# Kernel optimization log

Hardware: AMD Instinct MI355X
Metric: run time of the kernel (lower is better)

The kernel has to match this reference:

```python
import jax, jax.numpy as jnp
import numpy as np

EPS = 1e-5


def conv2d(x, w, stride=1, pad=1, b=None):
    out = jax.lax.conv_general_dilated(
        x, w, (stride, stride), [(pad, pad), (pad, pad)],
        dimension_numbers=('NCHW', 'OIHW', 'NCHW'))
    if b is not None:
        out = out + b[None, :, None, None]
    return out


def batchnorm(x, g, b):
    # training-mode BN (torch default): batch statistics over (N, H, W)
    m = x.mean((0, 2, 3), keepdims=True)
    v = x.var((0, 2, 3), keepdims=True)
    return (x - m) * jax.lax.rsqrt(v + EPS) * g[None, :, None, None] + b[None, :, None, None]


def deform(x, w_off):
    # ConvOffset2D: learn (B, 2C, H, W) offsets, bilinearly resample x per channel.
    B, C, H, W = x.shape
    off = conv2d(x, w_off, 1, 1)                 # (B, 2C, H, W)
    off = off.reshape(B * C, H * W, 2)           # matches torch row-major view to (B*C, H, W, 2)
    ii, jj = jnp.meshgrid(jnp.arange(H), jnp.arange(W), indexing='ij')
    grid = jnp.stack([ii, jj], -1).reshape(H * W, 2).astype(x.dtype)
    coords = off + grid[None]                    # absolute sample coords
    ci = jnp.clip(coords[..., 0], 0.0, H - 1)
    cj = jnp.clip(coords[..., 1], 0.0, W - 1)
    i0 = jnp.floor(ci)
    i1 = jnp.ceil(ci)
    j0 = jnp.floor(cj)
    j1 = jnp.ceil(cj)
    xf = x.reshape(B * C, H * W)

    def gather(iy, jx):
        idx = (iy * W + jx).astype(jnp.int32)
        return jnp.take_along_axis(xf, idx, axis=1)

    v00 = gather(i0, j0)
    v10 = gather(i1, j0)
    v01 = gather(i0, j1)
    v11 = gather(i1, j1)
    di = ci - i0
    dj = cj - j0
    top = v00 + di * (v10 - v00)   # interpolate along rows
    bot = v01 + di * (v11 - v01)
    out = top + dj * (bot - top)   # then along cols
    return out.reshape(B, C, H, W)


def setup_inputs() -> dict:
    key = jax.random.key(0)
    ks = jax.random.split(key, 24)
    f32 = jnp.float32
    d = {
        'x': jax.random.normal(ks[0], (64, 1, 112, 112), dtype=f32),
        'w11': jax.random.normal(ks[1], (32, 1, 3, 3), dtype=f32) * 0.1,
        'b11': jnp.zeros((32,), f32),
        'g11': jnp.ones((32,), f32),
        'be11': jnp.zeros((32,), f32),
        'woff12': jax.random.normal(ks[2], (64, 32, 3, 3), dtype=f32) * 0.01,
        'w12': jax.random.normal(ks[3], (64, 32, 3, 3), dtype=f32) * 0.1,
        'b12': jnp.zeros((64,), f32),
        'g12': jnp.ones((64,), f32),
        'be12': jnp.zeros((64,), f32),
        'woff21': jax.random.normal(ks[4], (128, 64, 3, 3), dtype=f32) * 0.01,
        'w21': jax.random.normal(ks[5], (128, 64, 3, 3), dtype=f32) * 0.1,
        'b21': jnp.zeros((128,), f32),
        'g21': jnp.ones((128,), f32),
        'be21': jnp.zeros((128,), f32),
        'woff22': jax.random.normal(ks[6], (256, 128, 3, 3), dtype=f32) * 0.01,
        'w22': jax.random.normal(ks[7], (128, 128, 3, 3), dtype=f32) * 0.1,
        'b22': jnp.zeros((128,), f32),
        'g22': jnp.ones((128,), f32),
        'be22': jnp.zeros((128,), f32),
        'wfc': jax.random.normal(ks[8], (10, 128), dtype=f32) * 0.1,
        'bfc': jnp.zeros((10,), f32),
    }
    return d


def reference(x, w11, b11, g11, be11, woff12, w12, b12, g12, be12,
              woff21, w21, b21, g21, be21, woff22, w22, b22, g22, be22,
              wfc, bfc):
    x = batchnorm(jax.nn.relu(conv2d(x, w11, 1, 1, b11)), g11, be11)
    x = deform(x, woff12)
    x = batchnorm(jax.nn.relu(conv2d(x, w12, 2, 1, b12)), g12, be12)
    x = deform(x, woff21)
    x = batchnorm(jax.nn.relu(conv2d(x, w21, 1, 1, b21)), g21, be21)
    x = deform(x, woff22)
    x = batchnorm(jax.nn.relu(conv2d(x, w22, 2, 1, b22)), g22, be22)
    x = x.mean((2, 3))                       # global avg pool -> (B, 128)
    logits = x @ wfc.T + bfc
    return jax.nn.softmax(logits, axis=1)
```

## Files before the change

### kernel.cpp

```cpp
#include <hip/hip_runtime.h>
#include <math.h>

#define BN_EPS 1e-5f

typedef unsigned short ushort_t;
typedef unsigned int uint_t;
typedef _Float16 half_t;
typedef __attribute__((ext_vector_type(8))) short short8;
typedef __attribute__((ext_vector_type(8))) _Float16 half8;
typedef __attribute__((ext_vector_type(4))) unsigned uint4v;
typedef __attribute__((ext_vector_type(2))) unsigned uint2v;
typedef __attribute__((ext_vector_type(16))) float floatx16;

__device__ __forceinline__ void split_bf16(float v, ushort_t& h, ushort_t& l) {
    unsigned u = __float_as_uint(v);
    float fhi = __uint_as_float(u & 0xFFFF0000u);
    h = (ushort_t)(u >> 16);
    l = (ushort_t)(__float_as_uint(v - fhi) >> 16);
}

__device__ __forceinline__ uint_t split_word(float v) {
    ushort_t h, l;
    split_bf16(v, h, l);
    return ((uint_t)h << 16) | (uint_t)l;
}

__device__ __forceinline__ float h2f_lo(uint_t u) {
    union { ushort_t s; half_t h; } cv; cv.s = (ushort_t)(u & 0xFFFFu);
    return (float)cv.h;
}
__device__ __forceinline__ float h2f_hi(uint_t u) {
    union { ushort_t s; half_t h; } cv; cv.s = (ushort_t)(u >> 16);
    return (float)cv.h;
}

__global__ __launch_bounds__(256) void prep_w_kernel(
    const float* __restrict__ w, ushort_t* __restrict__ hi,
    ushort_t* __restrict__ lo, int O, int I)
{
    int idx = blockIdx.x * 256 + threadIdx.x;
    int n = 9 * O * I;
    if (idx >= n) return;
    int i = idx % I;
    int rest = idx / I;
    int o = rest % O;
    int t = rest / O;
    float v = w[((size_t)o * I + i) * 9 + t];
    size_t d = ((((size_t)t * (O / 32) + (o >> 5)) * (I / 8) + (i >> 3)) * 32
                + (o & 31)) * 8 + (i & 7);
    split_bf16(v, hi[d], lo[d]);
}

__global__ __launch_bounds__(256) void prep_wf16_kernel(
    const float* __restrict__ w, half_t* __restrict__ o, int O, int I)
{
    int idx = blockIdx.x * 256 + threadIdx.x;
    int n = 9 * O * I;
    if (idx >= n) return;
    int i = idx % I;
    int rest = idx / I;
    int oo = rest % O;
    int t = rest / O;
    float v = w[((size_t)oo * I + i) * 9 + t];
    size_t d = ((((size_t)t * (O / 32) + (oo >> 5)) * (I / 8) + (i >> 3)) * 32
                + (oo & 31)) * 8 + (i & 7);
    o[d] = (half_t)v;
}

__global__ __launch_bounds__(256) void pack_af16_kernel(
    const float* __restrict__ x, const float* __restrict__ aff,
    half_t* __restrict__ xt, half_t* __restrict__ xl,
    int C, int HW, int total)
{
    int idx = blockIdx.x * 256 + threadIdx.x;
    if (idx >= total) return;
    int p = idx % HW;
    int rest = idx / HW;
    int cg = rest % (C / 8);
    int b  = rest / (C / 8);
    const float* xp = x + ((size_t)b * C + cg * 8) * HW + p;
    half8 hv;
    #pragma unroll
    for (int j = 0; j < 8; j++) {
        int c = cg * 8 + j;
        float v = fmaf(xp[(size_t)j * HW], aff[2 * c], aff[2 * c + 1]);
        hv[j] = (half_t)v;
        xl[((size_t)b * C + c) * HW + p] = hv[j];
    }
    size_t base = (size_t)b * C * HW + ((size_t)(p >> 5) * (C / 8) + cg) * 256
                + (size_t)(p & 31) * 8;
    *(half8*)(xt + base) = hv;
}

__global__ void bn_finalize_kernel(
    const float* __restrict__ stats, const float* __restrict__ g,
    const float* __restrict__ be, float inv_cnt, float* __restrict__ aff, int C)
{
    int c = threadIdx.x;
    if (c < C) {
        float m  = stats[c] * inv_cnt;
        float vv = stats[C + c] * inv_cnt - m * m;
        float sc = g[c] / sqrtf(vv + BN_EPS);
        aff[2 * c]     = sc;
        aff[2 * c + 1] = be[c] - m * sc;
    }
}

template<int W, int H, int CIN, int CO, int NT, int NZ>
__global__ __launch_bounds__(512, 4) void mfma_deform_g(
    const half_t* __restrict__ xt, const half_t* __restrict__ xl,
    const half_t* __restrict__ wf, uint_t* __restrict__ outp)
{
    constexpr int HWi = W * H;
    constexpr int KB  = CIN / 8;
    constexpr int TILES = HWi / 32;
    constexpr int XTB = (TILES + 7) / 8;
    constexpr int PER = XTB * NZ;
    constexpr int PITCH = 68;
    constexpr int QGH = HWi / 64;
    constexpr int NC2 = CIN / 16;
    constexpr int NCH = 9 * NT;
    constexpr int NPASS = (NCH + 7) / 8;
    constexpr int BUFB = NCH * 1024;
    constexpr size_t EPIB = 8 * (16 * PITCH * 8) + 8 * 1024;
    constexpr size_t LDSB = (2 * (size_t)BUFB > EPIB) ? 2 * (size_t)BUFB : EPIB;
    const half8 zero8 = {0, 0, 0, 0, 0, 0, 0, 0};

    __shared__ __align__(16) char ldsb[LDSB];

    const int tid  = threadIdx.x;
    const int wv   = tid >> 6;
    const int lane = tid & 63;
    const int l31  = lane & 31;
    const int kg   = lane >> 5;

    const int bid   = blockIdx.x;
    const int xcd   = bid & 7;
    const int s     = bid >> 3;
    const int kslot = s / PER;
    const int inner = s % PER;
    const int xti   = inner % XTB;
    const int zz    = inner / XTB;
    const int n0t   = zz * NT;
    const int b     = xcd * 8 + kslot;
    const int t0r   = xti * 8 + wv;
    const bool act  = t0r < TILES;
    const int t0    = act ? t0r : TILES - 1;

    const int mp = t0 * 32 + l31;
    const int py = mp / W, px = mp % W;
    const size_t xtb = (size_t)b * CIN * HWi;

    unsigned aoff[9];
    unsigned amask = 0;
    #pragma unroll
    for (int ki = 0; ki < 3; ki++) {
        #pragma unroll
        for (int kj = 0; kj < 3; kj++) {
            int t  = ki * 3 + kj;
            int iy = py + ki - 1, ix = px + kj - 1;
            bool v = (iy >= 0 && iy < H && ix >= 0 && ix < W);
            int ps = v ? iy * W + ix : 0;
            aoff[t] = (unsigned)((ps >> 5) * KB * 256 + (ps & 31) * 8);
            amask |= (v ? 1u : 0u) << t;
        }
    }

    floatx16 acc[NT];
    #pragma unroll
    for (int i = 0; i < NT; i++)
        #pragma unroll
        for (int j = 0; j < 16; j++) acc[i][j] = 0.f;

    auto stage = [&](int c2s, int buf) {
        #pragma unroll
        for (int it = 0; it < NPASS; it++) {
            int slot  = it * 8 + wv;
            int chunk = slot < NCH ? slot : slot - NCH;
            int t  = chunk / NT;
            int nt = chunk % NT;
            const half_t* src = wf
                + (((size_t)t * (CO / 32) + (n0t + nt)) * KB + (size_t)c2s * 2) * 256
                + lane * 8;
            __builtin_amdgcn_global_load_lds(
                (const __attribute__((address_space(1))) unsigned*)src,
                (__attribute__((address_space(3))) unsigned*)(ldsb + buf * BUFB + chunk * 1024),
                16, 0, 0);
        }
    };

    stage(0, 0);
    asm volatile("s_waitcnt vmcnt(0)" ::: "memory");
    __syncthreads();

    for (int c2 = 0; c2 < NC2; c2++) {
        const int cur = c2 & 1;
        if (c2 + 1 < NC2) stage(c2 + 1, cur ^ 1);
        const unsigned kb = c2 * 2 + kg;
        #pragma unroll
        for (int t = 0; t < 9; t++) {
            const size_t au = xtb + aoff[t] + (size_t)kb * 256;
            half8 a = *(const half8*)(xt + au);
            if (!((amask >> t) & 1u)) a = zero8;
            #pragma unroll
            for (int nt = 0; nt < NT; nt++) {
                const half8 bv = *(const half8*)(ldsb + cur * BUFB
                                 + (t * NT + nt) * 1024 + kg * 512 + l31 * 16);
                acc[nt] = __builtin_amdgcn_mfma_f32_32x32x16_f16(a, bv, acc[nt], 0, 0, 0);
            }
        }
        if (c2 + 1 < NC2) {
            asm volatile("s_waitcnt vmcnt(0)" ::: "memory");
            __syncthreads();
        }
    }

    __syncthreads();

    if (!act) return;

    float2* offw = (float2*)(ldsb + (size_t)wv * (16 * PITCH * 8));
    uint_t* stgw = (uint_t*)(ldsb + 8 * (16 * PITCH * 8) + (size_t)wv * 1024);
    const int qb  = (t0 & 1) * 16;
    const int qg0 = t0 >> 1;

    #pragma unroll
    for (int half = 0; half < NT / 2; half++) {
        #pragma unroll
        for (int ntl = 0; ntl < 2; ntl++) {
            const int gl = ntl * 32 + l31;
            #pragma unroll
            for (int t = 0; t < 8; t++) {
                int r2w = (t & 1) + 2 * kg + 4 * (t >> 1);
                offw[r2w * PITCH + gl] =
                    float2{acc[half * 2 + ntl][2 * t], acc[half * 2 + ntl][2 * t + 1]};
            }
        }
        asm volatile("s_waitcnt lgkmcnt(0)" ::: "memory");

        const int bc0 = n0t * 16 + half * 32;
        #pragma unroll
        for (int sc = 0; sc < 4; sc++) {
            const int r2 = lane & 15;
            #pragma unroll
            for (int sub = 0; sub < 4; sub++) {
                const int gl  = sc * 16 + sub * 4 + (lane >> 4);
                float2 od = offw[r2 * PITCH + gl];
                const int hlf = (lane >> 4) & 1;
                const int c   = bc0 + sc * 8 + sub * 2 + kg;
                const int q   = hlf * (HWi / 2) + t0 * 16 + r2;
                const int qi = q / W, qj = q % W;
                float ci_ = fminf(fmaxf(od.x + (float)qi, 0.f), (float)(H - 1));
                float cj_ = fminf(fmaxf(od.y + (float)qj, 0.f), (float)(W - 1));
                float i0f = floorf(ci_), j0f = floorf(cj_);
                int i0 = (int)i0f, i1 = (int)ceilf(ci_);
                int j0 = (int)j0f;
                const half_t* gp = xl + xtb + (size_t)c * HWi;
                uint_t u0 = *(const uint_t*)(gp + i0 * W + j0);
                uint_t u1 = *(const uint_t*)(gp + i1 * W + j0);
                float v00 = h2f_lo(u0), v01 = h2f_hi(u0);
                float v10 = h2f_lo(u1), v11 = h2f_hi(u1);
                float di = ci_ - i0f, dj = cj_ - j0f;
                float top = v00 + di * (v10 - v00);
                float bot = v01 + di * (v11 - v01);
                float res = top + dj * (bot - top);
                stgw[hlf * 128 + r2 * 8 + (sub * 2 + kg)] = split_word(res);
            }
            asm volatile("s_waitcnt lgkmcnt(0)" ::: "memory");
            const int cg = (bc0 >> 3) + sc;
            #pragma unroll
            for (int hlf = 0; hlf < 2; hlf++) {
                uint2v dd = *(const uint2v*)&stgw[hlf * 128 + 2 * lane];
                size_t dst = xtb + ((size_t)(hlf * QGH + qg0) * KB + cg) * 256
                           + (size_t)qb * 8 + 2 * lane;
                *(uint2v*)(outp + dst) = dd;
            }
        }
    }
}

template<int S, int W, int H, int CIN, int CO, int NT, int NZ>
__global__ __launch_bounds__(512, 4) void mfma_conv_g(
    const uint_t* __restrict__ xt,
    const ushort_t* __restrict__ wh, const ushort_t* __restrict__ wl,
    const float* __restrict__ bias, float* __restrict__ out)
{
    constexpr int Wo  = W / S, Ho = H / S;
    constexpr int HWo = Wo * Ho;
    constexpr int HWi = W * H;
    constexpr int KB  = CIN / 8;
    constexpr int TILES = (HWo + 31) / 32;
    constexpr int XTB = (TILES + 7) / 8;
    constexpr int PER = XTB * NZ;
    constexpr int NC2 = CIN / 16;
    constexpr int NCH = 9 * NT * 2;
    constexpr int NPASS = (NCH + 7) / 8;
    constexpr int BUFB = NCH * 1024;

    __shared__ __align__(16) char ldsb[2 * BUFB];

    const int tid  = threadIdx.x;
    const int wv   = tid >> 6;
    const int lane = tid & 63;
    const int l31  = lane & 31;
    const int kg   = lane >> 5;

    const int bid   = blockIdx.x;
    const int xcd   = bid & 7;
    const int s     = bid >> 3;
    const int kslot = s / PER;
    const int inner = s % PER;
    const int xti   = inner % XTB;
    const int zz    = inner / XTB;
    const int n0t   = zz * NT;
    const int b     = xcd * 8 + kslot;
    const int t0r   = xti * 8 + wv;
    const bool act  = t0r < TILES;
    const int t0    = act ? t0r : TILES - 1;

    const int mp  = t0 * 32 + l31;
    const int mpc = mp < HWo ? mp : HWo - 1;
    const int py  = mpc / Wo, px = mpc % Wo;
    const size_t xtb = (size_t)b * CIN * HWi;

    unsigned aoff[9];
    unsigned amask = 0;
    #pragma unroll
    for (int ki = 0; ki < 3; ki++) {
        #pragma unroll
        for (int kj = 0; kj < 3; kj++) {
            int t  = ki * 3 + kj;
            int iy = py * S + ki - 1, ix = px * S + kj - 1;
            bool v = (iy >= 0 && iy < H && ix >= 0 && ix < W);
            int ps = v ? iy * W + ix : 0;
            aoff[t] = (unsigned)((ps >> 5) * KB * 256 + (ps & 31) * 8);
            amask |= (v ? 1u : 0u) << t;
        }
    }

    floatx16 acc[NT];
    #pragma unroll
    for (int i = 0; i < NT; i++)
        #pragma unroll
        for (int j = 0; j < 16; j++) acc[i][j] = 0.f;

    auto stage = [&](int c2s, int buf) {
        #pragma unroll
        for (int it = 0; it < NPASS; it++) {
            int slot  = it * 8 + wv;
            int chunk = slot < NCH ? slot : slot - NCH;
            int plane = chunk & 1;
            int tn = chunk >> 1;
            int t  = tn / NT;
            int nt = tn % NT;
            const ushort_t* srcp = (plane ? wl : wh)
                + (((size_t)t * (CO / 32) + (n0t + nt)) * KB + (size_t)c2s * 2) * 256
                + lane * 8;
            __builtin_amdgcn_global_load_lds(
                (const __attribute__((address_space(1))) unsigned*)srcp,
                (__attribute__((address_space(3))) unsigned*)(ldsb + buf * BUFB + chunk * 1024),
                16, 0, 0);
        }
    };

    stage(0, 0);
    asm volatile("s_waitcnt vmcnt(0)" ::: "memory");
    __syncthreads();

    for (int c2 = 0; c2 < NC2; c2++) {
        const int cur = c2 & 1;
        if (c2 + 1 < NC2) stage(c2 + 1, cur ^ 1);
        const unsigned kb = c2 * 2 + kg;
        #pragma unroll
        for (int t = 0; t < 9; t++) {
            const size_t au = xtb + aoff[t] + (size_t)kb * 256;
            uint4v w0 = *(const uint4v*)(xt + au);
            uint4v w1 = *(const uint4v*)(xt + au + 4);
            if (!((amask >> t) & 1u)) {
                w0 = uint4v{0, 0, 0, 0};
                w1 = uint4v{0, 0, 0, 0};
            }
            union { short8 s; uint_t u[4]; } uh, ul;
            uh.u[0] = (w0.x >> 16) | (w0.y & 0xFFFF0000u);
            uh.u[1] = (w0.z >> 16) | (w0.w & 0xFFFF0000u);
            uh.u[2] = (w1.x >> 16) | (w1.y & 0xFFFF0000u);
            uh.u[3] = (w1.z >> 16) | (w1.w & 0xFFFF0000u);
            ul.u[0] = (w0.x & 0xFFFFu) | (w0.y << 16);
            ul.u[1] = (w0.z & 0xFFFFu) | (w0.w << 16);
            ul.u[2] = (w1.x & 0xFFFFu) | (w1.y << 16);
            ul.u[3] = (w1.z & 0xFFFFu) | (w1.w << 16);
            short8 ah = uh.s, al = ul.s;
            #pragma unroll
            for (int nt = 0; nt < NT; nt++) {
                const char* bb = ldsb + cur * BUFB
                               + ((t * NT + nt) * 2) * 1024 + kg * 512 + l31 * 16;
                short8 bh = *(const short8*)bb;
                short8 bl = *(const short8*)(bb + 1024);
                floatx16 a = acc[nt];
                a = __builtin_amdgcn_mfma_f32_32x32x16_bf16(ah, bh, a, 0, 0, 0);
                a = __builtin_amdgcn_mfma_f32_32x32x16_bf16(ah, bl, a, 0, 0, 0);
                a = __builtin_amdgcn_mfma_f32_32x32x16_bf16(al, bh, a, 0, 0, 0);
                acc[nt] = a;
            }
        }
        if (c2 + 1 < NC2) {
            asm volatile("s_waitcnt vmcnt(0)" ::: "memory");
            __syncthreads();
        }
    }

    if (!act) return;

    #pragma unroll
    for (int nt = 0; nt < NT; nt++) {
        int co = (n0t + nt) * 32 + l31;
        float bv = bias[co];
        #pragma unroll
        for (int reg = 0; reg < 16; reg++) {
            int row = (reg & 3) + 8 * (reg >> 2) + 4 * kg;
            int p   = t0 * 32 + row;
            if (p < HWo)
                out[((size_t)b * CO + co) * HWo + p] = fmaxf(acc[nt][reg] + bv, 0.f);
        }
    }
}

template<int STRIDE>
__global__ __launch_bounds__(256) void conv3x3_kernel(
    const float* __restrict__ in, const float* __restrict__ wgt,
    const float* __restrict__ bias, float* __restrict__ out,
    int B, int Cin, int H, int W, int Cout, int Ho, int Wo, int do_relu)
{
    constexpr int TILE = 28;
    constexpr int PR   = (TILE - 1) * STRIDE + 3;
    constexpr int PADW = (STRIDE == 1) ? 32 : 60;
    constexpr int COPB = 8;
    constexpr int RW   = STRIDE + 3;
    __shared__ float patch[PR * PADW];

    int cpg  = Cout / COPB;
    int bz   = blockIdx.z;
    int cog  = bz % cpg;
    int b    = bz / cpg;
    int co0  = cog * COPB;
    int tid  = threadIdx.x;
    int oy0  = blockIdx.y * TILE, ox0 = blockIdx.x * TILE;
    int iy0  = oy0 * STRIDE - 1,  ix0 = ox0 * STRIDE - 1;

    bool active = tid < 196;
    int ty = tid / 14, tx = tid % 14;
    int py = oy0 + 2 * ty, px = ox0 + 2 * tx;

    float acc[COPB][4];
    #pragma unroll
    for (int i = 0; i < COPB; i++) {
        float bv = bias ? bias[co0 + i] : 0.f;
        #pragma unroll
        for (int j = 0; j < 4; j++) acc[i][j] = bv;
    }

    const size_t HW = (size_t)H * W;
    for (int ci = 0; ci < Cin; ci++) {
        const float* ip = in + ((size_t)b * Cin + ci) * HW;
        for (int t = tid; t < PR * PADW; t += 256) {
            int sy = t / PADW, sx = t % PADW;
            float v = 0.f;
            int gy = iy0 + sy, gx = ix0 + sx;
            if (sx < PR && gy >= 0 && gy < H && gx >= 0 && gx < W)
                v = ip[(size_t)gy * W + gx];
            patch[t] = v;
        }
        __syncthreads();
        if (active) {
            float r[RW][RW];
            #pragma unroll
            for (int rr = 0; rr < RW; rr++) {
                int rowbase = (2 * ty * STRIDE + rr) * PADW + 2 * tx * STRIDE;
                if (STRIDE == 1) {
                    float2 a = *(const float2*)&patch[rowbase];
                    float2 c = *(const float2*)&patch[rowbase + 2];
                    r[rr][0] = a.x; r[rr][1] = a.y; r[rr][2] = c.x; r[rr][3] = c.y;
                } else {
                    float4 a = *(const float4*)&patch[rowbase];
                    r[rr][0] = a.x; r[rr][1] = a.y; r[rr][2] = a.z; r[rr][3] = a.w;
                    r[rr][4] = patch[rowbase + 4];
                }
            }
            const float* wb = wgt + ((size_t)co0 * Cin + ci) * 9;
            #pragma unroll
            for (int i = 0; i < COPB; i++) {
                const float* wp = wb + (size_t)i * Cin * 9;
                #pragma unroll
                for (int ki = 0; ki < 3; ki++)
                    #pragma unroll
                    for (int kj = 0; kj < 3; kj++) {
                        float w = wp[ki * 3 + kj];
                        acc[i][0] = fmaf(r[ki][kj],                   w, acc[i][0]);
                        acc[i][1] = fmaf(r[ki][kj + STRIDE],          w, acc[i][1]);
                        acc[i][2] = fmaf(r[ki + STRIDE][kj],          w, acc[i][2]);
                        acc[i][3] = fmaf(r[ki + STRIDE][kj + STRIDE], w, acc[i][3]);
                    }
            }
        }
        __syncthreads();
    }
    if (active) {
        #pragma unroll
        for (int rr = 0; rr < 2; rr++) {
            #pragma unroll
            for (int cc = 0; cc < 2; cc++) {
                int oy = py + rr, ox = px + cc;
                if (oy < Ho && ox < Wo) {
                    #pragma unroll
                    for (int i = 0; i < COPB; i++) {
                        float v = acc[i][rr * 2 + cc];
                        if (do_relu) v = fmaxf(v, 0.f);
                        out[(((size_t)b * Cout + co0 + i) * Ho + oy) * Wo + ox] = v;
                    }
                }
            }
        }
    }
}

__global__ __launch_bounds__(256) void bn_stats_kernel(
    const float* __restrict__ x, float* __restrict__ stats,
    int B, int C, int HW)
{
    int c = blockIdx.x;
    long long cnt = (long long)B * HW;
    long long step = (long long)gridDim.y * blockDim.x;
    float s = 0.f, s2 = 0.f;
    for (long long t = (long long)blockIdx.y * blockDim.x + threadIdx.x; t < cnt; t += step) {
        int b  = (int)(t / HW);
        int sp = (int)(t % HW);
        float v = x[((size_t)b * C + c) * (size_t)HW + sp];
        s += v; s2 += v * v;
    }
    for (int off = 32; off; off >>= 1) {
        s  += __shfl_down(s, off);
        s2 += __shfl_down(s2, off);
    }
    __shared__ float ls[4], ls2[4];
    int wave = threadIdx.x >> 6, lane = threadIdx.x & 63;
    if (lane == 0) { ls[wave] = s; ls2[wave] = s2; }
    __syncthreads();
    if (threadIdx.x == 0) {
        float ts = 0.f, ts2 = 0.f;
        for (int i = 0; i < 4; i++) { ts += ls[i]; ts2 += ls2[i]; }
        atomicAdd(&stats[c], ts);
        atomicAdd(&stats[C + c], ts2);
    }
}

__global__ void zero_kernel(float* __restrict__ p, int n)
{
    int i = blockIdx.x * blockDim.x + threadIdx.x;
    if (i < n) p[i] = 0.f;
}

__global__ __launch_bounds__(256) void pool_kernel(
    const float* __restrict__ x, const float* __restrict__ stats,
    const float* __restrict__ g, const float* __restrict__ be,
    float inv_cnt, float* __restrict__ out, int C, int HW)
{
    int bc = blockIdx.x;
    int c  = bc % C;
    const float* xp = x + (size_t)bc * HW;
    float s = 0.f;
    for (int i = threadIdx.x; i < HW; i += blockDim.x) s += xp[i];
    for (int off = 32; off; off >>= 1) s += __shfl_down(s, off);
    __shared__ float ls[4];
    int wave = threadIdx.x >> 6, lane = threadIdx.x & 63;
    if (lane == 0) ls[wave] = s;
    __syncthreads();
    if (threadIdx.x == 0) {
        float t = 0.f;
        for (int i = 0; i < 4; i++) t += ls[i];
        float mean = t / (float)HW;
        float m  = stats[c] * inv_cnt;
        float vv = stats[C + c] * inv_cnt - m * m;
        float sc = g[c] / sqrtf(vv + BN_EPS);
        float sh = be[c] - m * sc;
        out[bc] = mean * sc + sh;
    }
}

__global__ __launch_bounds__(128) void fc_softmax_kernel(
    const float* __restrict__ pool, const float* __restrict__ wfc,
    const float* __restrict__ bfc, float* __restrict__ out)
{
    int b = blockIdx.x;
    __shared__ float row[128];
    __shared__ float logits[10];
    int tid = threadIdx.x;
    row[tid] = pool[b * 128 + tid];
    __syncthreads();
    if (tid < 10) {
        float s = bfc[tid];
        for (int k = 0; k < 128; k++) s = fmaf(row[k], wfc[tid * 128 + k], s);
        logits[tid] = s;
    }
    __syncthreads();
    if (tid < 10) {
        float mx = logits[0];
        for (int i = 1; i < 10; i++) mx = fmaxf(mx, logits[i]);
        float sum = 0.f;
        for (int i = 0; i < 10; i++) sum += expf(logits[i] - mx);
        out[b * 10 + tid] = expf(logits[tid] - mx) / sum;
    }
}

extern "C" void kernel_launch(void* const* d_in, const int* in_sizes, int n_in,
                              void* d_out, int out_size, void* d_ws, size_t ws_size,
                              hipStream_t stream)
{
    const float* x      = (const float*)d_in[0];
    const float* w11    = (const float*)d_in[1];
    const float* b11    = (const float*)d_in[2];
    const float* g11    = (const float*)d_in[3];
    const float* be11   = (const float*)d_in[4];
    const float* woff12 = (const float*)d_in[5];
    const float* w12    = (const float*)d_in[6];
    const float* b12    = (const float*)d_in[7];
    const float* g12    = (const float*)d_in[8];
    const float* be12   = (const float*)d_in[9];
    const float* woff21 = (const float*)d_in[10];
    const float* w21    = (const float*)d_in[11];
    const float* b21    = (const float*)d_in[12];
    const float* g21    = (const float*)d_in[13];
    const float* be21   = (const float*)d_in[14];
    const float* woff22 = (const float*)d_in[15];
    const float* w22    = (const float*)d_in[16];
    const float* b22    = (const float*)d_in[17];
    const float* g22    = (const float*)d_in[18];
    const float* be22   = (const float*)d_in[19];
    const float* wfc    = (const float*)d_in[20];
    const float* bfc    = (const float*)d_in[21];
    float* out = (float*)d_out;

    float* ws    = (float*)d_ws;
    const size_t SZ_B = 25690112;

    float*  R0f = ws;
    uint_t* R0u = (uint_t*)R0f;
    half_t* R0h = (half_t*)R0f;
    half_t* R0l = R0h + SZ_B;
    float* stats = R0f + SZ_B;
    float* aff   = stats + 512;
    float* poolb = aff + 512;
    uint_t* R1u = (uint_t*)(poolb + 8192);
    float*  R1f = (float*)R1u;
    half_t* R1h = (half_t*)R1u;
    half_t* R1l = R1h + SZ_B;
    ushort_t* warena = (ushort_t*)(R1u + SZ_B);
    const size_t W12 = 9 * 64 * 32;
    const size_t W21 = 9 * 128 * 64;
    const size_t W22c = 9 * 128 * 128;
    const size_t W12o = 9 * 64 * 32;
    const size_t W21o = 9 * 128 * 64;
    ushort_t* wc12h = warena;          ushort_t* wc12l = wc12h + W12;
    ushort_t* wc21h = wc12l + W12;     ushort_t* wc21l = wc21h + W21;
    ushort_t* wc22h = wc21l + W21;     ushort_t* wc22l = wc22h + W22c;
    half_t* wpf12 = (half_t*)(wc22l + W22c);
    half_t* wpf21 = wpf12 + W12o;
    half_t* wpf22 = wpf21 + W21o;

    const int B = 64;

    prep_w_kernel<<<(9*64*32   + 255)/256, 256, 0, stream>>>(w12, wc12h, wc12l, 64, 32);
    prep_w_kernel<<<(9*128*64  + 255)/256, 256, 0, stream>>>(w21, wc21h, wc21l, 128, 64);
    prep_w_kernel<<<(9*128*128 + 255)/256, 256, 0, stream>>>(w22, wc22h, wc22l, 128, 128);
    prep_wf16_kernel<<<(9*64*32   + 255)/256, 256, 0, stream>>>(woff12, wpf12, 64, 32);
    prep_wf16_kernel<<<(9*128*64  + 255)/256, 256, 0, stream>>>(woff21, wpf21, 128, 64);
    prep_wf16_kernel<<<(9*256*128 + 255)/256, 256, 0, stream>>>(woff22, wpf22, 256, 128);

    conv3x3_kernel<1><<<dim3(4, 4, B * (32 / 8)), 256, 0, stream>>>(
        x, w11, b11, R0f, B, 1, 112, 112, 32, 112, 112, 1);
    zero_kernel<<<2, 256, 0, stream>>>(stats, 512);
    bn_stats_kernel<<<dim3(32, 64), 256, 0, stream>>>(R0f, stats, B, 32, 12544);
    bn_finalize_kernel<<<1, 256, 0, stream>>>(stats, g11, be11, 1.f/(64.f*12544.f), aff, 32);

    pack_af16_kernel<<<(B*4*12544 + 255)/256, 256, 0, stream>>>(
        R0f, aff, R1h, R1l, 32, 12544, B*4*12544);
    mfma_deform_g<112, 112, 32, 64, 2, 1>
        <<<dim3(64 * 49), 512, 0, stream>>>(R1h, R1l, wpf12, R0u);

    mfma_conv_g<2, 112, 112, 32, 64, 2, 1>
        <<<dim3(64 * 13), 512, 0, stream>>>(R0u, wc12h, wc12l, b12, R1f);
    zero_kernel<<<2, 256, 0, stream>>>(stats, 512);
    bn_stats_kernel<<<dim3(64, 64), 256, 0, stream>>>(R1f, stats, B, 64, 3136);
    bn_finalize_kernel<<<1, 256, 0, stream>>>(stats, g12, be12, 1.f/(64.f*3136.f), aff, 64);

    pack_af16_kernel<<<(B*8*3136 + 255)/256, 256, 0, stream>>>(
        R1f, aff, R0h, R0l, 64, 3136, B*8*3136);
    mfma_deform_g<56, 56, 64, 128, 4, 1>
        <<<dim3(64 * 13), 512, 0, stream>>>(R0h, R0l, wpf21, R1u);

    mfma_conv_g<1, 56, 56, 64, 128, 2, 2>
        <<<dim3(64 * 26), 512, 0, stream>>>(R1u, wc21h, wc21l, b21, R0f);
    zero_kernel<<<2, 256, 0, stream>>>(stats, 512);
    bn_stats_kernel<<<dim3(128, 64), 256, 0, stream>>>(R0f, stats, B, 128, 3136);
    bn_finalize_kernel<<<1, 256, 0, stream>>>(stats, g21, be21, 1.f/(64.f*3136.f), aff, 128);

    pack_af16_kernel<<<(B*16*3136 + 255)/256, 256, 0, stream>>>(
        R0f, aff, R1h, R1l, 128, 3136, B*16*3136);
    mfma_deform_g<56, 56, 128, 256, 4, 2>
        <<<dim3(64 * 26), 512, 0, stream>>>(R1h, R1l, wpf22, R0u);

    mfma_conv_g<2, 56, 56, 128, 128, 2, 2>
        <<<dim3(64 * 8), 512, 0, stream>>>(R0u, wc22h, wc22l, b22, R1f);
    zero_kernel<<<2, 256, 0, stream>>>(stats, 512);
    bn_stats_kernel<<<dim3(128, 64), 256, 0, stream>>>(R1f, stats, B, 128, 784);

    pool_kernel<<<B * 128, 256, 0, stream>>>(
        R1f, stats, g22, be22, 1.f/(64.f*784.f), poolb, 128, 784);
    fc_softmax_kernel<<<B, 128, 0, stream>>>(poolb, wfc, bfc, out);
}
```

Baseline: 1.041 ms.

## Fuse BN statistics reduction into conv epilogues, drop separate bn_stats passes

Each conv kernel (first direct conv and the MFMA convs) now accumulates per-channel sum and sum-of-squares of its ReLU output in registers and LDS, then atomically adds them to a global stats buffer. This removes four bn_stats kernels, each of which re-read the full activation tensor, plus the per-layer zero kernels (replaced by one upfront zero). The cost is extra epilogue work, a barrier and more global atomics per block, and float atomics make the summation order non-deterministic.

```diff
diff --git a/kernel.cpp b/kernel.cpp
--- a/kernel.cpp
+++ b/kernel.cpp
@@ -283,7 +283,8 @@
 __global__ __launch_bounds__(512, 4) void mfma_conv_g(
     const uint_t* __restrict__ xt,
     const ushort_t* __restrict__ wh, const ushort_t* __restrict__ wl,
-    const float* __restrict__ bias, float* __restrict__ out)
+    const float* __restrict__ bias, float* __restrict__ out,
+    float* __restrict__ stats)
 {
     constexpr int Wo  = W / S, Ho = H / S;
     constexpr int HWo = Wo * Ho;
@@ -298,6 +299,7 @@
     constexpr int BUFB = NCH * 1024;
 
     __shared__ __align__(16) char ldsb[2 * BUFB];
+    __shared__ float sred[NT * 32 * 2];
 
     const int tid  = threadIdx.x;
     const int wv   = tid >> 6;
@@ -337,6 +339,8 @@
             amask |= (v ? 1u : 0u) << t;
         }
     }
+
+    for (int i = tid; i < NT * 64; i += 512) sred[i] = 0.f;
 
     floatx16 acc[NT];
     #pragma unroll
@@ -409,6 +413,46 @@
         }
     }
 
+    float sv[NT], sv2[NT];
+    #pragma unroll
+    for (int nt = 0; nt < NT; nt++) {
+        int co = (n0t + nt) * 32 + l31;
+        float bv = bias[co];
+        float ss = 0.f, ss2 = 0.f;
+        if (act) {
+            #pragma unroll
+            for (int reg = 0; reg < 16; reg++) {
+                int row = (reg & 3) + 8 * (reg >> 2) + 4 * kg;
+                int p   = t0 * 32 + row;
+                if (p < HWo) {
+                    float v = fmaxf(acc[nt][reg] + bv, 0.f);
+                    ss += v; ss2 += v * v;
+                }
+            }
+        }
+        sv[nt] = ss; sv2[nt] = ss2;
+    }
+    #pragma unroll
+    for (int nt = 0; nt < NT; nt++) {
+        sv[nt]  += __shfl_down(sv[nt], 32);
+        sv2[nt] += __shfl_down(sv2[nt], 32);
+    }
+    __syncthreads();
+    if (kg == 0) {
+        #pragma unroll
+        for (int nt = 0; nt < NT; nt++) {
+            atomicAdd(&sred[(nt * 32 + l31) * 2],     sv[nt]);
+            atomicAdd(&sred[(nt * 32 + l31) * 2 + 1], sv2[nt]);
+        }
+    }
+    __syncthreads();
+    if (tid < NT * 32) {
+        int nt = tid >> 5, l = tid & 31;
+        int co = (n0t + nt) * 32 + l;
+        atomicAdd(&stats[co],      sred[tid * 2]);
+        atomicAdd(&stats[CO + co], sred[tid * 2 + 1]);
+    }
+
     if (!act) return;
 
     #pragma unroll
@@ -429,6 +473,7 @@
 __global__ __launch_bounds__(256) void conv3x3_kernel(
     const float* __restrict__ in, const float* __restrict__ wgt,
     const float* __restrict__ bias, float* __restrict__ out,
+    float* __restrict__ stats,
     int B, int Cin, int H, int W, int Cout, int Ho, int Wo, int do_relu)
 {
     constexpr int TILE = 28;
@@ -437,6 +482,7 @@
     constexpr int COPB = 8;
     constexpr int RW   = STRIDE + 3;
     __shared__ float patch[PR * PADW];
+    __shared__ float sred[COPB][2];
 
     int cpg  = Cout / COPB;
     int bz   = blockIdx.z;
@@ -450,6 +496,8 @@
     bool active = tid < 196;
     int ty = tid / 14, tx = tid % 14;
     int py = oy0 + 2 * ty, px = ox0 + 2 * tx;
+
+    if (tid < COPB * 2) ((float*)sred)[tid] = 0.f;
 
     float acc[COPB][4];
     #pragma unroll
@@ -506,50 +554,29 @@
     }
     if (active) {
         #pragma unroll
-        for (int rr = 0; rr < 2; rr++) {
-            #pragma unroll
-            for (int cc = 0; cc < 2; cc++) {
-                int oy = py + rr, ox = px + cc;
-                if (oy < Ho && ox < Wo) {
-                    #pragma unroll
-                    for (int i = 0; i < COPB; i++) {
+        for (int i = 0; i < COPB; i++) {
+            float ss = 0.f, ss2 = 0.f;
+            #pragma unroll
+            for (int rr = 0; rr < 2; rr++) {
+                #pragma unroll
+                for (int cc = 0; cc < 2; cc++) {
+                    int oy = py + rr, ox = px + cc;
+                    if (oy < Ho && ox < Wo) {
                         float v = acc[i][rr * 2 + cc];
                         if (do_relu) v = fmaxf(v, 0.f);
                         out[(((size_t)b * Cout + co0 + i) * Ho + oy) * Wo + ox] = v;
+                        ss += v; ss2 += v * v;
                     }
                 }
             }
-        }
-    }
-}
-
-__global__ __launch_bounds__(256) void bn_stats_kernel(
-    const float* __restrict__ x, float* __restrict__ stats,
-    int B, int C, int HW)
-{
-    int c = blockIdx.x;
-    long long cnt = (long long)B * HW;
-    long long step = (long long)gridDim.y * blockDim.x;
-    float s = 0.f, s2 = 0.f;
-    for (long long t = (long long)blockIdx.y * blockDim.x + threadIdx.x; t < cnt; t += step) {
-        int b  = (int)(t / HW);
-        int sp = (int)(t % HW);
-        float v = x[((size_t)b * C + c) * (size_t)HW + sp];
-        s += v; s2 += v * v;
-    }
-    for (int off = 32; off; off >>= 1) {
-        s  += __shfl_down(s, off);
-        s2 += __shfl_down(s2, off);
-    }
-    __shared__ float ls[4], ls2[4];
-    int wave = threadIdx.x >> 6, lane = threadIdx.x & 63;
-    if (lane == 0) { ls[wave] = s; ls2[wave] = s2; }
-    __syncthreads();
-    if (threadIdx.x == 0) {
-        float ts = 0.f, ts2 = 0.f;
-        for (int i = 0; i < 4; i++) { ts += ls[i]; ts2 += ls2[i]; }
-        atomicAdd(&stats[c], ts);
-        atomicAdd(&stats[C + c], ts2);
+            atomicAdd(&sred[i][0], ss);
+            atomicAdd(&sred[i][1], ss2);
+        }
+    }
+    __syncthreads();
+    if (tid < COPB) {
+        atomicAdd(&stats[co0 + tid],        sred[tid][0]);
+        atomicAdd(&stats[Cout + co0 + tid], sred[tid][1]);
     }
 }
 
@@ -646,8 +673,12 @@
     uint_t* R0u = (uint_t*)R0f;
     half_t* R0h = (half_t*)R0f;
     half_t* R0l = R0h + SZ_B;
-    float* stats = R0f + SZ_B;
-    float* aff   = stats + 512;
+    float* statsA = R0f + SZ_B;
+    float* stats0 = statsA;
+    float* stats1 = statsA + 512;
+    float* stats2 = statsA + 1024;
+    float* stats3 = statsA + 1536;
+    float* aff   = statsA + 2048;
     float* poolb = aff + 512;
     uint_t* R1u = (uint_t*)(poolb + 8192);
     float*  R1f = (float*)R1u;
@@ -668,6 +699,7 @@
 
     const int B = 64;
 
+    zero_kernel<<<8, 256, 0, stream>>>(statsA, 2048);
     prep_w_kernel<<<(9*64*32   + 255)/256, 256, 0, stream>>>(w12, wc12h, wc12l, 64, 32);
     prep_w_kernel<<<(9*128*64  + 255)/256, 256, 0, stream>>>(w21, wc21h, wc21l, 128, 64);
     prep_w_kernel<<<(9*128*128 + 255)/256, 256, 0, stream>>>(w22, wc22h, wc22l, 128, 128);
@@ -676,10 +708,8 @@
     prep_wf16_kernel<<<(9*256*128 + 255)/256, 256, 0, stream>>>(woff22, wpf22, 256, 128);
 
     conv3x3_kernel<1><<<dim3(4, 4, B * (32 / 8)), 256, 0, stream>>>(
-        x, w11, b11, R0f, B, 1, 112, 112, 32, 112, 112, 1);
-    zero_kernel<<<2, 256, 0, stream>>>(stats, 512);
-    bn_stats_kernel<<<dim3(32, 64), 256, 0, stream>>>(R0f, stats, B, 32, 12544);
-    bn_finalize_kernel<<<1, 256, 0, stream>>>(stats, g11, be11, 1.f/(64.f*12544.f), aff, 32);
+        x, w11, b11, R0f, stats0, B, 1, 112, 112, 32, 112, 112, 1);
+    bn_finalize_kernel<<<1, 256, 0, stream>>>(stats0, g11, be11, 1.f/(64.f*12544.f), aff, 32);
 
     pack_af16_kernel<<<(B*4*12544 + 255)/256, 256, 0, stream>>>(
         R0f, aff, R1h, R1l, 32, 12544, B*4*12544);
@@ -687,10 +717,8 @@
         <<<dim3(64 * 49), 512, 0, stream>>>(R1h, R1l, wpf12, R0u);
 
     mfma_conv_g<2, 112, 112, 32, 64, 2, 1>
-        <<<dim3(64 * 13), 512, 0, stream>>>(R0u, wc12h, wc12l, b12, R1f);
-    zero_kernel<<<2, 256, 0, stream>>>(stats, 512);
-    bn_stats_kernel<<<dim3(64, 64), 256, 0, stream>>>(R1f, stats, B, 64, 3136);
-    bn_finalize_kernel<<<1, 256, 0, stream>>>(stats, g12, be12, 1.f/(64.f*3136.f), aff, 64);
+        <<<dim3(64 * 13), 512, 0, stream>>>(R0u, wc12h, wc12l, b12, R1f, stats1);
+    bn_finalize_kernel<<<1, 256, 0, stream>>>(stats1, g12, be12, 1.f/(64.f*3136.f), aff, 64);
 
     pack_af16_kernel<<<(B*8*3136 + 255)/256, 256, 0, stream>>>(
         R1f, aff, R0h, R0l, 64, 3136, B*8*3136);
@@ -698,10 +726,8 @@
         <<<dim3(64 * 13), 512, 0, stream>>>(R0h, R0l, wpf21, R1u);
 
     mfma_conv_g<1, 56, 56, 64, 128, 2, 2>
-        <<<dim3(64 * 26), 512, 0, stream>>>(R1u, wc21h, wc21l, b21, R0f);
-    zero_kernel<<<2, 256, 0, stream>>>(stats, 512);
-    bn_stats_kernel<<<dim3(128, 64), 256, 0, stream>>>(R0f, stats, B, 128, 3136);
-    bn_finalize_kernel<<<1, 256, 0, stream>>>(stats, g21, be21, 1.f/(64.f*3136.f), aff, 128);
+        <<<dim3(64 * 26), 512, 0, stream>>>(R1u, wc21h, wc21l, b21, R0f, stats2);
+    bn_finalize_kernel<<<1, 256, 0, stream>>>(stats2, g21, be21, 1.f/(64.f*3136.f), aff, 128);
 
     pack_af16_kernel<<<(B*16*3136 + 255)/256, 256, 0, stream>>>(
         R0f, aff, R1h, R1l, 128, 3136, B*16*3136);
@@ -709,11 +735,9 @@
         <<<dim3(64 * 26), 512, 0, stream>>>(R1h, R1l, wpf22, R0u);
 
     mfma_conv_g<2, 56, 56, 128, 128, 2, 2>
-        <<<dim3(64 * 8), 512, 0, stream>>>(R0u, wc22h, wc22l, b22, R1f);
-    zero_kernel<<<2, 256, 0, stream>>>(stats, 512);
-    bn_stats_kernel<<<dim3(128, 64), 256, 0, stream>>>(R1f, stats, B, 128, 784);
+        <<<dim3(64 * 8), 512, 0, stream>>>(R0u, wc22h, wc22l, b22, R1f, stats3);
 
     pool_kernel<<<B * 128, 256, 0, stream>>>(
-        R1f, stats, g22, be22, 1.f/(64.f*784.f), poolb, 128, 784);
+        R1f, stats3, g22, be22, 1.f/(64.f*784.f), poolb, 128, 784);
     fc_softmax_kernel<<<B, 128, 0, stream>>>(poolb, wfc, bfc, out);
 }
```

Result: no change. 1.058 ms (+1.6%).
